# Performance work log

Measured on AMD Instinct MI355X. Metric: run time of the kernel, lower is better.

## Reference

```python
import jax, jax.numpy as jnp
import numpy as np

ALPHA = 1.0
BETA = 0.25
NUM_EMBEDS = 8192
EMBED_DIM = 512
B, T = 32, 256


def setup_inputs() -> dict:
    key = jax.random.key(0)
    k1, k2 = jax.random.split(key)
    z_e = jax.random.normal(k1, (B, EMBED_DIM, T), dtype=jnp.float32)
    codebook = jax.random.normal(k2, (NUM_EMBEDS, EMBED_DIM), dtype=jnp.float32)
    return {"z_e": z_e, "codebook": codebook}


def reference(z_e, codebook):
    # z_e: (b, d, t) -> (b, t, d)
    z = jnp.transpose(z_e, (0, 2, 1))
    b, t, d = z.shape
    flat = z.reshape(-1, d)  # (N, d), N = b*t

    # squared euclidean distances to every codebook vector: (N, K)
    dists = (
        jnp.sum(flat * flat, axis=1, keepdims=True)
        + jnp.sum(codebook * codebook, axis=1)
        - 2.0 * flat @ codebook.T
    )
    idx = jnp.argmin(dists, axis=1)  # (N,)

    # codebook lookup (equivalent to one-hot @ codebook)
    z_q = codebook[idx].reshape(b, t, d)

    # commitment loss (codebook is EMA-updated, so only e_latent term)
    e_latent_loss = jnp.mean((jax.lax.stop_gradient(z_q) - z) ** 2)
    vq_loss = ALPHA * BETA * e_latent_loss

    # straight-through estimator
    z_q_st = z + jax.lax.stop_gradient(z_q - z)
    z_q_out = jnp.transpose(z_q_st, (0, 2, 1))  # back to (b, d, t)

    # perplexity from mean one-hot assignment probabilities
    counts = jnp.zeros((codebook.shape[0],), dtype=jnp.float32).at[idx].add(1.0)
    avg_probs = counts / flat.shape[0]
    perplexity = jnp.exp(-jnp.sum(avg_probs * jnp.log(avg_probs + 1e-10)))

    return z_q_out, vq_loss, perplexity
```

## Files before the change

### kernel.cpp

```cpp
#include <hip/hip_runtime.h>
#include <stdint.h>

typedef _Float16 half8 __attribute__((ext_vector_type(8)));
typedef float floatx16 __attribute__((ext_vector_type(16)));

#define ALPHA_ 1.0f
#define BETA_ 0.25f
#define NUM_EMBEDS 8192
#define EMBED_DIM 512
#define B_ 32
#define T_ 256
#define N_TOK (B_ * T_)


__global__ void cnorm_kernel(const float* __restrict__ cb, float* __restrict__ cnorm) {
    int row = blockIdx.x * 4 + (threadIdx.x >> 6);
    int lane = threadIdx.x & 63;
    const float4* p = (const float4*)(cb + (size_t)row * EMBED_DIM);
    float4 v0 = p[lane * 2], v1 = p[lane * 2 + 1];
    float s = v0.x * v0.x + v0.y * v0.y + v0.z * v0.z + v0.w * v0.w +
              v1.x * v1.x + v1.y * v1.y + v1.z * v1.z + v1.w * v1.w;
    for (int m = 32; m; m >>= 1) s += __shfl_xor(s, m, 64);
    if (lane == 0) cnorm[row] = s;
}

#define TK_BLK 128
#define TN_BLK 128
#define KCHUNK 1024
#define NCOL (KCHUNK / TK_BLK)
#define KSPLIT (NUM_EMBEDS / KCHUNK)
#define RS 20

__device__ __forceinline__ uint32_t pack2(float x) {
    _Float16 h = (_Float16)x;
    float hf = (float)h;
    _Float16 m = (_Float16)((x - hf) * 2048.0f);
    return (uint32_t)__builtin_bit_cast(unsigned short, h) |
           ((uint32_t)__builtin_bit_cast(unsigned short, m) << 16);
}

union H8 { uint32_t u[4]; half8 h; };

__device__ __forceinline__ void unpack_frag(const uint32_t* p, half8& hh, half8& mm) {
    uint4 u0 = *(const uint4*)p;
    uint4 u1 = *(const uint4*)(p + 4);
    H8 a, b;
    a.u[0] = __builtin_amdgcn_perm(u0.y, u0.x, 0x05040100u);
    a.u[1] = __builtin_amdgcn_perm(u0.w, u0.z, 0x05040100u);
    a.u[2] = __builtin_amdgcn_perm(u1.y, u1.x, 0x05040100u);
    a.u[3] = __builtin_amdgcn_perm(u1.w, u1.z, 0x05040100u);
    b.u[0] = __builtin_amdgcn_perm(u0.y, u0.x, 0x07060302u);
    b.u[1] = __builtin_amdgcn_perm(u0.w, u0.z, 0x07060302u);
    b.u[2] = __builtin_amdgcn_perm(u1.y, u1.x, 0x07060302u);
    b.u[3] = __builtin_amdgcn_perm(u1.w, u1.z, 0x07060302u);
    hh = a.h; mm = b.h;
}

__global__ __launch_bounds__(256, 2) void argmin_kernel(
    const float* __restrict__ z, const float* __restrict__ cb,
    const float* __restrict__ cnorm, unsigned long long* __restrict__ wmin) {
    __shared__ uint32_t As[TK_BLK * RS];
    __shared__ uint32_t Bs[TN_BLK * RS];
    const int tid = threadIdx.x;
    const int lane = tid & 63;
    const int wv = tid >> 6;
    const int wp = wv >> 1;
    const int wq = wv & 1;
    const int l31 = lane & 31;
    const int half = lane >> 5;

    const int n0 = blockIdx.x * TN_BLK;
    const int bb = n0 >> 8;
    const int t0 = n0 & 255;
    const int kbase = blockIdx.y * KCHUNK;

    const int a_code = tid >> 1;
    const int a_dh = tid & 1;
    const int b_t = tid & 127;
    const int b_dgrp = tid >> 7;

    unsigned long long best[2] = {~0ULL, ~0ULL};

    for (int col = 0; col < NCOL; ++col) {
        const int kb = kbase + col * TK_BLK;
        floatx16 acc1[2][2], acc2[2][2];
#pragma unroll
        for (int pi = 0; pi < 2; ++pi)
#pragma unroll
            for (int qi = 0; qi < 2; ++qi)
#pragma unroll
                for (int r = 0; r < 16; ++r) { acc1[pi][qi][r] = 0.0f; acc2[pi][qi][r] = 0.0f; }

        for (int step = 0; step < 33; ++step) {
            const int d0 = step * 16;
            uint32_t apack[8], bpack[8];
            if (step < 32) {
                const float* srcA = cb + (size_t)(kb + a_code) * EMBED_DIM + d0 + a_dh * 8;
                float4 v0 = *(const float4*)srcA;
                float4 v1 = *(const float4*)(srcA + 4);
                apack[0] = pack2(v0.x); apack[1] = pack2(v0.y);
                apack[2] = pack2(v0.z); apack[3] = pack2(v0.w);
                apack[4] = pack2(v1.x); apack[5] = pack2(v1.y);
                apack[6] = pack2(v1.z); apack[7] = pack2(v1.w);
                const float* srcB = z + ((size_t)bb * EMBED_DIM + d0 + b_dgrp * 8) * T_ + t0 + b_t;
#pragma unroll
                for (int j = 0; j < 8; ++j)
                    bpack[j] = pack2(-2.0f * srcB[(size_t)j * T_]);
            } else {
#pragma unroll
                for (int j = 0; j < 8; ++j) { apack[j] = 0u; bpack[j] = 0u; }
                if (a_dh == 0) apack[0] = pack2(cnorm[kb + a_code]);
                if (b_dgrp == 0) bpack[0] = 0x00003C00u;
            }
            __syncthreads();
            *(uint4*)&As[a_code * RS + a_dh * 8 + 0] = make_uint4(apack[0], apack[1], apack[2], apack[3]);
            *(uint4*)&As[a_code * RS + a_dh * 8 + 4] = make_uint4(apack[4], apack[5], apack[6], apack[7]);
            *(uint4*)&Bs[b_t * RS + b_dgrp * 8 + 0] = make_uint4(bpack[0], bpack[1], bpack[2], bpack[3]);
            *(uint4*)&Bs[b_t * RS + b_dgrp * 8 + 4] = make_uint4(bpack[4], bpack[5], bpack[6], bpack[7]);
            __syncthreads();

            half8 Ah[2], Am[2], Bh[2], Bm[2];
#pragma unroll
            for (int pi = 0; pi < 2; ++pi)
                unpack_frag(&As[(wp * 64 + pi * 32 + l31) * RS + half * 8], Ah[pi], Am[pi]);
#pragma unroll
            for (int qi = 0; qi < 2; ++qi)
                unpack_frag(&Bs[(wq * 64 + qi * 32 + l31) * RS + half * 8], Bh[qi], Bm[qi]);
#pragma unroll
            for (int pi = 0; pi < 2; ++pi)
#pragma unroll
                for (int qi = 0; qi < 2; ++qi) {
                    acc1[pi][qi] = __builtin_amdgcn_mfma_f32_32x32x16_f16(Ah[pi], Bh[qi], acc1[pi][qi], 0, 0, 0);
                    acc2[pi][qi] = __builtin_amdgcn_mfma_f32_32x32x16_f16(Ah[pi], Bm[qi], acc2[pi][qi], 0, 0, 0);
                    acc2[pi][qi] = __builtin_amdgcn_mfma_f32_32x32x16_f16(Am[pi], Bh[qi], acc2[pi][qi], 0, 0, 0);
                }
        }

#pragma unroll
        for (int qi = 0; qi < 2; ++qi)
#pragma unroll
            for (int pi = 0; pi < 2; ++pi)
#pragma unroll
                for (int r = 0; r < 16; ++r) {
                    float s = acc1[pi][qi][r] + acc2[pi][qi][r] * (1.0f / 2048.0f);
                    int code = kb + wp * 64 + pi * 32 + (r & 3) + ((r >> 2) << 3) + (half << 2);
                    uint32_t u = __float_as_uint(s);
                    u = (u & 0x80000000u) ? ~u : (u | 0x80000000u);
                    unsigned long long key = ((unsigned long long)u << 32) | (unsigned long long)(unsigned)code;
                    if (key < best[qi]) best[qi] = key;
                }
    }

#pragma unroll
    for (int qi = 0; qi < 2; ++qi) {
        unsigned long long o = __shfl_xor(best[qi], 32, 64);
        if (o < best[qi]) best[qi] = o;
        if (half == 0) {
            int token = n0 + wq * 64 + qi * 32 + l31;
            atomicMin(&wmin[token], best[qi]);
        }
    }
}

__global__ void gather_kernel(const float* __restrict__ z, const float* __restrict__ cb,
                              const unsigned long long* __restrict__ wmin,
                              float* __restrict__ out, int* __restrict__ counts,
                              float* __restrict__ sse_acc) {
    __shared__ unsigned int sIdx[64];
    __shared__ float red[4];
    const int tid = threadIdx.x;
    const int n0 = blockIdx.x * 64;
    const int b = n0 >> 8;
    const int t0 = n0 & 255;
    if (tid < 64) {
        unsigned int idx = (unsigned int)(wmin[n0 + tid] & 0xffffffffULL);
        sIdx[tid] = idx;
        atomicAdd(&counts[idx], 1);
    }
    __syncthreads();
    const int w = tid >> 6;
    const int lane = tid & 63;
    const float* crow = cb + (size_t)sIdx[lane] * EMBED_DIM;
    const size_t base = ((size_t)b * EMBED_DIM) * T_ + (size_t)(t0 + lane);
    float sse = 0.f;
    for (int d = w; d < EMBED_DIM; d += 4) {
        float v = crow[d];
        size_t o = base + (size_t)d * T_;
        float diff = v - z[o];
        out[o] = v;
        sse += diff * diff;
    }
    for (int m = 32; m; m >>= 1) sse += __shfl_xor(sse, m, 64);
    if (lane == 0) red[w] = sse;
    __syncthreads();
    if (tid == 0) atomicAdd(sse_acc, red[0] + red[1] + red[2] + red[3]);
}

__global__ void finalize_kernel(const int* __restrict__ counts,
                                const float* __restrict__ sse_acc,
                                float* __restrict__ out) {
    __shared__ float red[4];
    const int tid = threadIdx.x;
    float e = 0.f;
    for (int k = tid; k < NUM_EMBEDS; k += 256) {
        float p = (float)counts[k] * (1.0f / (float)N_TOK);
        e += p * logf(p + 1e-10f);
    }
    for (int m = 32; m; m >>= 1) e += __shfl_xor(e, m, 64);
    if ((tid & 63) == 0) red[tid >> 6] = e;
    __syncthreads();
    if (tid == 0) {
        float ent = red[0] + red[1] + red[2] + red[3];
        size_t off = (size_t)B_ * EMBED_DIM * T_;
        out[off + 0] = (ALPHA_ * BETA_) * sse_acc[0] / (float)((size_t)N_TOK * EMBED_DIM);
        out[off + 1] = expf(-ent);
    }
}

extern "C" void kernel_launch(void* const* d_in, const int* in_sizes, int n_in,
                              void* d_out, int out_size, void* d_ws, size_t ws_size,
                              hipStream_t stream) {
    const float* z = (const float*)d_in[0];
    const float* cb = (const float*)d_in[1];
    float* out = (float*)d_out;
    char* ws = (char*)d_ws;
    unsigned long long* wmin = (unsigned long long*)ws;
    float* cnorm = (float*)(ws + 65536);
    int* counts = (int*)(ws + 98304);
    float* sse = (float*)(ws + 131072);

    hipMemsetAsync(wmin, 0xFF, NUM_EMBEDS * sizeof(unsigned long long), stream);
    hipMemsetAsync(counts, 0, NUM_EMBEDS * sizeof(int) + sizeof(float), stream);

    cnorm_kernel<<<NUM_EMBEDS / 4, 256, 0, stream>>>(cb, cnorm);
    argmin_kernel<<<dim3(N_TOK / TN_BLK, KSPLIT), 256, 0, stream>>>(z, cb, cnorm, wmin);
    gather_kernel<<<N_TOK / 64, 256, 0, stream>>>(z, cb, wmin, out, counts, sse);
    finalize_kernel<<<1, 256, 0, stream>>>(counts, sse, out);
}
```

Baseline: 435.6 us.

## Pre-pack operands to fp16 hi/lo planes and stream via global_load_lds

Adds pre-pass kernels that split the codebook and the transposed, pre-scaled z into separate fp16 high and residual planes. The argmin GEMM then copies 16-byte chunks straight from global memory into LDS with global_load_lds, prefetching the next K-step while the current one computes. The codebook norm is now added in the epilogue instead of through an extra 33rd MFMA step. This removes repeated per-block fp32-to-fp16 conversion and the strided z loads from the hot loop. In exchange it costs extra global traffic for the packed buffers (about 32 MB of workspace), and the single-buffer prefetch requires a second barrier per step.

```diff
diff --git a/kernel.cpp b/kernel.cpp
--- a/kernel.cpp
+++ b/kernel.cpp
@@ -10,122 +10,121 @@
 #define EMBED_DIM 512
 #define B_ 32
 #define T_ 256
-#define N_TOK (B_ * T_)
-
-
-__global__ void cnorm_kernel(const float* __restrict__ cb, float* __restrict__ cnorm) {
+#define N_TOK 8192
+
+
+typedef __attribute__((address_space(1))) const void ga_void;
+typedef __attribute__((address_space(3))) void ls_void;
+__device__ __forceinline__ void gl_lds16(const void* g, void* l) {
+    __builtin_amdgcn_global_load_lds((ga_void*)g, (ls_void*)l, 16, 0, 0);
+}
+
+__global__ void pack_cb_kernel(const float* __restrict__ cb, _Float16* __restrict__ h,
+                               _Float16* __restrict__ m, float* __restrict__ cnorm) {
     int row = blockIdx.x * 4 + (threadIdx.x >> 6);
     int lane = threadIdx.x & 63;
-    const float4* p = (const float4*)(cb + (size_t)row * EMBED_DIM);
-    float4 v0 = p[lane * 2], v1 = p[lane * 2 + 1];
-    float s = v0.x * v0.x + v0.y * v0.y + v0.z * v0.z + v0.w * v0.w +
-              v1.x * v1.x + v1.y * v1.y + v1.z * v1.z + v1.w * v1.w;
-    for (int m = 32; m; m >>= 1) s += __shfl_xor(s, m, 64);
+    const float* src = cb + (size_t)row * EMBED_DIM + lane * 8;
+    float4 v0 = *(const float4*)src;
+    float4 v1 = *(const float4*)(src + 4);
+    float x[8] = {v0.x, v0.y, v0.z, v0.w, v1.x, v1.y, v1.z, v1.w};
+    half8 hh, mm;
+    float s = 0.f;
+#pragma unroll
+    for (int j = 0; j < 8; ++j) {
+        s += x[j] * x[j];
+        _Float16 hv = (_Float16)x[j];
+        hh[j] = hv;
+        mm[j] = (_Float16)((x[j] - (float)hv) * 2048.0f);
+    }
+    *(half8*)(h + (size_t)row * EMBED_DIM + lane * 8) = hh;
+    *(half8*)(m + (size_t)row * EMBED_DIM + lane * 8) = mm;
+#pragma unroll
+    for (int d = 32; d; d >>= 1) s += __shfl_xor(s, d, 64);
     if (lane == 0) cnorm[row] = s;
 }
 
-#define TK_BLK 128
-#define TN_BLK 128
-#define KCHUNK 1024
-#define NCOL (KCHUNK / TK_BLK)
-#define KSPLIT (NUM_EMBEDS / KCHUNK)
-#define RS 20
-
-__device__ __forceinline__ uint32_t pack2(float x) {
-    _Float16 h = (_Float16)x;
-    float hf = (float)h;
-    _Float16 m = (_Float16)((x - hf) * 2048.0f);
-    return (uint32_t)__builtin_bit_cast(unsigned short, h) |
-           ((uint32_t)__builtin_bit_cast(unsigned short, m) << 16);
-}
-
-union H8 { uint32_t u[4]; half8 h; };
-
-__device__ __forceinline__ void unpack_frag(const uint32_t* p, half8& hh, half8& mm) {
-    uint4 u0 = *(const uint4*)p;
-    uint4 u1 = *(const uint4*)(p + 4);
-    H8 a, b;
-    a.u[0] = __builtin_amdgcn_perm(u0.y, u0.x, 0x05040100u);
-    a.u[1] = __builtin_amdgcn_perm(u0.w, u0.z, 0x05040100u);
-    a.u[2] = __builtin_amdgcn_perm(u1.y, u1.x, 0x05040100u);
-    a.u[3] = __builtin_amdgcn_perm(u1.w, u1.z, 0x05040100u);
-    b.u[0] = __builtin_amdgcn_perm(u0.y, u0.x, 0x07060302u);
-    b.u[1] = __builtin_amdgcn_perm(u0.w, u0.z, 0x07060302u);
-    b.u[2] = __builtin_amdgcn_perm(u1.y, u1.x, 0x07060302u);
-    b.u[3] = __builtin_amdgcn_perm(u1.w, u1.z, 0x07060302u);
-    hh = a.h; mm = b.h;
+__global__ void pack_z_kernel(const float* __restrict__ z, _Float16* __restrict__ h,
+                              _Float16* __restrict__ m) {
+    int tid = threadIdx.x;
+    int lane = tid & 63, ds = tid >> 6;
+    int b = blockIdx.x >> 2;
+    int t = ((blockIdx.x & 3) << 6) + lane;
+    size_t n = (size_t)b * T_ + t;
+    for (int g = 0; g < 16; ++g) {
+        int d0 = g * 32 + ds * 8;
+        const float* src = z + ((size_t)b * EMBED_DIM + d0) * T_ + t;
+        half8 hh, mm;
+#pragma unroll
+        for (int j = 0; j < 8; ++j) {
+            float x = -2.0f * src[(size_t)j * T_];
+            _Float16 hv = (_Float16)x;
+            hh[j] = hv;
+            mm[j] = (_Float16)((x - (float)hv) * 2048.0f);
+        }
+        *(half8*)(h + n * EMBED_DIM + d0) = hh;
+        *(half8*)(m + n * EMBED_DIM + d0) = mm;
+    }
 }
 
 __global__ __launch_bounds__(256, 2) void argmin_kernel(
-    const float* __restrict__ z, const float* __restrict__ cb,
+    const _Float16* __restrict__ cb_h, const _Float16* __restrict__ cb_m,
+    const _Float16* __restrict__ zt_h, const _Float16* __restrict__ zt_m,
     const float* __restrict__ cnorm, unsigned long long* __restrict__ wmin) {
-    __shared__ uint32_t As[TK_BLK * RS];
-    __shared__ uint32_t Bs[TN_BLK * RS];
+    __shared__ _Float16 smem[8192];
     const int tid = threadIdx.x;
     const int lane = tid & 63;
     const int wv = tid >> 6;
-    const int wp = wv >> 1;
-    const int wq = wv & 1;
     const int l31 = lane & 31;
-    const int half = lane >> 5;
-
-    const int n0 = blockIdx.x * TN_BLK;
-    const int bb = n0 >> 8;
-    const int t0 = n0 & 255;
-    const int kbase = blockIdx.y * KCHUNK;
-
-    const int a_code = tid >> 1;
-    const int a_dh = tid & 1;
-    const int b_t = tid & 127;
-    const int b_dgrp = tid >> 7;
-
-    unsigned long long best[2] = {~0ULL, ~0ULL};
-
-    for (int col = 0; col < NCOL; ++col) {
-        const int kb = kbase + col * TK_BLK;
+    const int hf = lane >> 5;
+    const int wp = wv >> 1, wq = wv & 1;
+    const int n0 = blockIdx.x * 128;
+    const int kbase = blockIdx.y * 1024;
+
+    const _Float16* gplane = (wv == 0) ? cb_h : (wv == 1) ? cb_m : (wv == 2) ? zt_h : zt_m;
+    const size_t gbase0 = ((wv < 2) ? (size_t)kbase : (size_t)n0) * EMBED_DIM +
+                          (size_t)(lane >> 1) * EMBED_DIM + (size_t)(lane & 1) * 8;
+    _Float16* lreg = &smem[wv * 2048];
+
+    const int fro = l31 * 16 + hf * 8;
+
+    unsigned long long best0 = ~0ULL, best1 = ~0ULL;
+
+    for (int col = 0; col < 8; ++col) {
+        const int kb = kbase + (col << 7);
+        const _Float16* g = gplane + gbase0 + ((wv < 2) ? (size_t)(col << 7) * EMBED_DIM : 0);
+
         floatx16 acc1[2][2], acc2[2][2];
 #pragma unroll
         for (int pi = 0; pi < 2; ++pi)
 #pragma unroll
             for (int qi = 0; qi < 2; ++qi)
 #pragma unroll
-                for (int r = 0; r < 16; ++r) { acc1[pi][qi][r] = 0.0f; acc2[pi][qi][r] = 0.0f; }
-
-        for (int step = 0; step < 33; ++step) {
-            const int d0 = step * 16;
-            uint32_t apack[8], bpack[8];
-            if (step < 32) {
-                const float* srcA = cb + (size_t)(kb + a_code) * EMBED_DIM + d0 + a_dh * 8;
-                float4 v0 = *(const float4*)srcA;
-                float4 v1 = *(const float4*)(srcA + 4);
-                apack[0] = pack2(v0.x); apack[1] = pack2(v0.y);
-                apack[2] = pack2(v0.z); apack[3] = pack2(v0.w);
-                apack[4] = pack2(v1.x); apack[5] = pack2(v1.y);
-                apack[6] = pack2(v1.z); apack[7] = pack2(v1.w);
-                const float* srcB = z + ((size_t)bb * EMBED_DIM + d0 + b_dgrp * 8) * T_ + t0 + b_t;
-#pragma unroll
-                for (int j = 0; j < 8; ++j)
-                    bpack[j] = pack2(-2.0f * srcB[(size_t)j * T_]);
-            } else {
-#pragma unroll
-                for (int j = 0; j < 8; ++j) { apack[j] = 0u; bpack[j] = 0u; }
-                if (a_dh == 0) apack[0] = pack2(cnorm[kb + a_code]);
-                if (b_dgrp == 0) bpack[0] = 0x00003C00u;
+                for (int r = 0; r < 16; ++r) { acc1[pi][qi][r] = 0.f; acc2[pi][qi][r] = 0.f; }
+
+#pragma unroll
+        for (int i = 0; i < 4; ++i)
+            gl_lds16(g + (size_t)(i * 32) * EMBED_DIM, lreg + i * 512);
+        __syncthreads();
+
+        for (int step = 0; step < 32; ++step) {
+            half8 Ah[2], Am[2], Bh[2], Bm[2];
+#pragma unroll
+            for (int pi = 0; pi < 2; ++pi) {
+                Ah[pi] = *(const half8*)&smem[(wp << 10) + (pi << 9) + fro];
+                Am[pi] = *(const half8*)&smem[2048 + (wp << 10) + (pi << 9) + fro];
+            }
+#pragma unroll
+            for (int qi = 0; qi < 2; ++qi) {
+                Bh[qi] = *(const half8*)&smem[4096 + (wq << 10) + (qi << 9) + fro];
+                Bm[qi] = *(const half8*)&smem[6144 + (wq << 10) + (qi << 9) + fro];
             }
             __syncthreads();
-            *(uint4*)&As[a_code * RS + a_dh * 8 + 0] = make_uint4(apack[0], apack[1], apack[2], apack[3]);
-            *(uint4*)&As[a_code * RS + a_dh * 8 + 4] = make_uint4(apack[4], apack[5], apack[6], apack[7]);
-            *(uint4*)&Bs[b_t * RS + b_dgrp * 8 + 0] = make_uint4(bpack[0], bpack[1], bpack[2], bpack[3]);
-            *(uint4*)&Bs[b_t * RS + b_dgrp * 8 + 4] = make_uint4(bpack[4], bpack[5], bpack[6], bpack[7]);
-            __syncthreads();
-
-            half8 Ah[2], Am[2], Bh[2], Bm[2];
-#pragma unroll
-            for (int pi = 0; pi < 2; ++pi)
-                unpack_frag(&As[(wp * 64 + pi * 32 + l31) * RS + half * 8], Ah[pi], Am[pi]);
-#pragma unroll
-            for (int qi = 0; qi < 2; ++qi)
-                unpack_frag(&Bs[(wq * 64 + qi * 32 + l31) * RS + half * 8], Bh[qi], Bm[qi]);
+            if (step < 31) {
+                const _Float16* gs = g + ((step + 1) << 4);
+#pragma unroll
+                for (int i = 0; i < 4; ++i)
+                    gl_lds16(gs + (size_t)(i * 32) * EMBED_DIM, lreg + i * 512);
+            }
 #pragma unroll
             for (int pi = 0; pi < 2; ++pi)
 #pragma unroll
@@ -134,30 +133,40 @@
                     acc2[pi][qi] = __builtin_amdgcn_mfma_f32_32x32x16_f16(Ah[pi], Bm[qi], acc2[pi][qi], 0, 0, 0);
                     acc2[pi][qi] = __builtin_amdgcn_mfma_f32_32x32x16_f16(Am[pi], Bh[qi], acc2[pi][qi], 0, 0, 0);
                 }
+            __syncthreads();
         }
 
 #pragma unroll
-        for (int qi = 0; qi < 2; ++qi)
-#pragma unroll
-            for (int pi = 0; pi < 2; ++pi)
-#pragma unroll
-                for (int r = 0; r < 16; ++r) {
-                    float s = acc1[pi][qi][r] + acc2[pi][qi][r] * (1.0f / 2048.0f);
-                    int code = kb + wp * 64 + pi * 32 + (r & 3) + ((r >> 2) << 3) + (half << 2);
+        for (int pi = 0; pi < 2; ++pi)
+#pragma unroll
+            for (int r = 0; r < 16; ++r) {
+                int code = kb + (wp << 6) + (pi << 5) + (r & 3) + ((r >> 2) << 3) + (hf << 2);
+                float cnv = cnorm[code];
+                {
+                    float s = cnv + acc1[pi][0][r] + acc2[pi][0][r] * (1.0f / 2048.0f);
                     uint32_t u = __float_as_uint(s);
                     u = (u & 0x80000000u) ? ~u : (u | 0x80000000u);
-                    unsigned long long key = ((unsigned long long)u << 32) | (unsigned long long)(unsigned)code;
-                    if (key < best[qi]) best[qi] = key;
+                    unsigned long long key = ((unsigned long long)u << 32) | (unsigned)code;
+                    if (key < best0) best0 = key;
                 }
-    }
-
-#pragma unroll
-    for (int qi = 0; qi < 2; ++qi) {
-        unsigned long long o = __shfl_xor(best[qi], 32, 64);
-        if (o < best[qi]) best[qi] = o;
-        if (half == 0) {
-            int token = n0 + wq * 64 + qi * 32 + l31;
-            atomicMin(&wmin[token], best[qi]);
+                {
+                    float s = cnv + acc1[pi][1][r] + acc2[pi][1][r] * (1.0f / 2048.0f);
+                    uint32_t u = __float_as_uint(s);
+                    u = (u & 0x80000000u) ? ~u : (u | 0x80000000u);
+                    unsigned long long key = ((unsigned long long)u << 32) | (unsigned)code;
+                    if (key < best1) best1 = key;
+                }
+            }
+    }
+
+    {
+        unsigned long long o = __shfl_xor(best0, 32, 64);
+        if (o < best0) best0 = o;
+        o = __shfl_xor(best1, 32, 64);
+        if (o < best1) best1 = o;
+        if (hf == 0) {
+            atomicMin(&wmin[n0 + (wq << 6) + l31], best0);
+            atomicMin(&wmin[n0 + (wq << 6) + 32 + l31], best1);
         }
     }
 }
@@ -228,12 +237,17 @@
     float* cnorm = (float*)(ws + 65536);
     int* counts = (int*)(ws + 98304);
     float* sse = (float*)(ws + 131072);
+    _Float16* cb_h = (_Float16*)(ws + (1ull << 20));
+    _Float16* cb_m = (_Float16*)(ws + (9ull << 20));
+    _Float16* zt_h = (_Float16*)(ws + (17ull << 20));
+    _Float16* zt_m = (_Float16*)(ws + (25ull << 20));
 
     hipMemsetAsync(wmin, 0xFF, NUM_EMBEDS * sizeof(unsigned long long), stream);
     hipMemsetAsync(counts, 0, NUM_EMBEDS * sizeof(int) + sizeof(float), stream);
 
-    cnorm_kernel<<<NUM_EMBEDS / 4, 256, 0, stream>>>(cb, cnorm);
-    argmin_kernel<<<dim3(N_TOK / TN_BLK, KSPLIT), 256, 0, stream>>>(z, cb, cnorm, wmin);
+    pack_cb_kernel<<<NUM_EMBEDS / 4, 256, 0, stream>>>(cb, cb_h, cb_m, cnorm);
+    pack_z_kernel<<<(B_ * T_) / 64, 256, 0, stream>>>(z, zt_h, zt_m);
+    argmin_kernel<<<dim3(N_TOK / 128, NUM_EMBEDS / 1024), 256, 0, stream>>>(cb_h, cb_m, zt_h, zt_m, cnorm, wmin);
     gather_kernel<<<N_TOK / 64, 256, 0, stream>>>(z, cb, wmin, out, counts, sse);
     finalize_kernel<<<1, 256, 0, stream>>>(counts, sse, out);
 }
```

Measured after the change: 427.1 us. Within noise of the previous version (-1.9%).
